# Kernel tuning notes

Measured on AMD Instinct MI355X. Metric: run time of the kernel, lower is better.

## Reference

```python
import jax, jax.numpy as jnp
import numpy as np

E = 500_000   # edges
N = 100_000   # nodes
Q = 256       # queries
N_REL = 200
R = 2 * N_REL + 1  # relation table rows (401)
D = 64        # in_dim
A = 64        # attn_dim
O = 64        # out_dim


def setup_inputs() -> dict:
    key = jax.random.key(0)
    ks = jax.random.split(key, 16)
    s = 1.0 / np.sqrt(D)
    # edges columns: [query_idx, head_ent, rel, tail_ent, sub_node, obj_node]
    col_q = jax.random.randint(ks[0], (E, 1), 0, Q)
    col_h = jax.random.randint(ks[1], (E, 1), 0, N)
    col_r = jax.random.randint(ks[2], (E, 1), 0, R)
    col_t = jax.random.randint(ks[3], (E, 1), 0, N)
    col_s = jax.random.randint(ks[4], (E, 1), 0, N)
    col_o = jax.random.randint(ks[5], (E, 1), 0, N)
    edges = jnp.concatenate([col_q, col_h, col_r, col_t, col_s, col_o], axis=1)
    return {
        "q_sub": jax.random.randint(ks[6], (Q,), 0, N),
        "q_emb": jax.random.normal(ks[7], (Q, D), dtype=jnp.float32),
        "rela_embed": jax.random.normal(ks[8], (R, D), dtype=jnp.float32),
        "hidden": jax.random.normal(ks[9], (N, D), dtype=jnp.float32),
        "edges": edges,
        "n_nodes": N,
        "Ws_W": jax.random.normal(ks[10], (A, D), dtype=jnp.float32) * s,
        "Ws_b": jnp.zeros((A,), dtype=jnp.float32),
        "Wr_W": jax.random.normal(ks[11], (A, D), dtype=jnp.float32) * s,
        "Wq_W": jax.random.normal(ks[12], (A, D), dtype=jnp.float32) * s,
        "Wqr_W": jax.random.normal(ks[13], (A, D), dtype=jnp.float32) * s,
        "wa_W": jax.random.normal(ks[14], (1, A), dtype=jnp.float32) * s,
        "wa_b": jnp.zeros((1,), dtype=jnp.float32),
        "Wh_W": jax.random.normal(ks[15], (O, D), dtype=jnp.float32) * s,
    }


def reference(q_sub, q_emb, rela_embed, hidden, edges, n_nodes,
              Ws_W, Ws_b, Wr_W, Wq_W, Wqr_W, wa_W, wa_b, Wh_W):
    # sample_flag == 0 path of GNNLayer.forward (use_lama_rel == 1, act = identity)
    sub = edges[:, 4]
    rel = edges[:, 2]
    obj = edges[:, 5]
    hs = hidden[sub]            # [E, D] gather
    hr = rela_embed[rel]        # [E, D] gather
    h_qr = q_emb[edges[:, 0]]   # [E, D] gather
    # attention MLP: sigmoid(w_alpha(ReLU(Ws hs + Wr hr + Wq hqr + Wqr (hr*hqr))))
    pre = (jnp.einsum('ed,ad->ea', hs, Ws_W) + Ws_b
           + jnp.einsum('ed,ad->ea', hr, Wr_W)
           + jnp.einsum('ed,ad->ea', h_qr, Wq_W)
           + jnp.einsum('ed,ad->ea', hr * h_qr, Wqr_W))
    alpha = jax.nn.sigmoid(jnp.einsum('ea,oa->eo', jax.nn.relu(pre), wa_W) + wa_b)  # [E,1]
    message = alpha * (hs * hr)                                # [E, D]
    message_agg = jax.ops.segment_sum(message, obj, num_segments=n_nodes)  # [N, D] scatter-sum
    hidden_new = jnp.einsum('nd,od->no', message_agg, Wh_W)    # act = identity
    return hidden_new, alpha
```

## Files before the change

kernel.cpp:

```cpp
#include <hip/hip_runtime.h>
#include <hip/hip_bf16.h>

#define EDGES  500000
#define NNODES 100000
#define QN     256
#define RN     401
#define DD     64
#define AA     64
#define OO     64

typedef __attribute__((ext_vector_type(8))) short short8;
typedef __attribute__((ext_vector_type(2))) short short2v;
typedef __attribute__((ext_vector_type(4))) float f32x4;
typedef __attribute__((ext_vector_type(2))) float f32x2;

__device__ inline unsigned short f2bf(float f) {
    union { float f; unsigned int u; } v; v.f = f;
    unsigned int u = v.u;
    u += 0x7FFFu + ((u >> 16) & 1u);
    return (unsigned short)(u >> 16);
}

__device__ inline f32x2 bfpair2f(unsigned int u) {
    union { unsigned int i; float f; } lo, hi;
    lo.i = u << 16;
    hi.i = u & 0xFFFF0000u;
    f32x2 r; r[0] = lo.f; r[1] = hi.f; return r;
}

__device__ inline short8 load8_cvt(const float* __restrict__ p) {
    f32x4 x0 = ((const f32x4*)p)[0];
    f32x4 x1 = ((const f32x4*)p)[1];
    short8 r;
    r[0] = (short)f2bf(x0[0]); r[1] = (short)f2bf(x0[1]);
    r[2] = (short)f2bf(x0[2]); r[3] = (short)f2bf(x0[3]);
    r[4] = (short)f2bf(x1[0]); r[5] = (short)f2bf(x1[1]);
    r[6] = (short)f2bf(x1[2]); r[7] = (short)f2bf(x1[3]);
    return r;
}

__device__ inline short8 load8_cvt_prod(const float* __restrict__ pa,
                                        const float* __restrict__ pb) {
    f32x4 a0 = ((const f32x4*)pa)[0];
    f32x4 a1 = ((const f32x4*)pa)[1];
    f32x4 b0 = ((const f32x4*)pb)[0];
    f32x4 b1 = ((const f32x4*)pb)[1];
    short8 r;
    r[0] = (short)f2bf(a0[0]*b0[0]); r[1] = (short)f2bf(a0[1]*b0[1]);
    r[2] = (short)f2bf(a0[2]*b0[2]); r[3] = (short)f2bf(a0[3]*b0[3]);
    r[4] = (short)f2bf(a1[0]*b1[0]); r[5] = (short)f2bf(a1[1]*b1[1]);
    r[6] = (short)f2bf(a1[2]*b1[2]); r[7] = (short)f2bf(a1[3]*b1[3]);
    return r;
}

__device__ inline void atomic_pk_add_bf16(short* addr, short2v v) {
#if __has_builtin(__builtin_amdgcn_global_atomic_fadd_v2bf16)
    __builtin_amdgcn_global_atomic_fadd_v2bf16(
        (__attribute__((address_space(1))) short2v*)addr, v);
#else
    asm volatile("global_atomic_pk_add_bf16 %0, %1, off"
                 :: "v"(addr), "v"(v) : "memory");
#endif
}

__global__ void k_xs(const float* __restrict__ hidden,
                     const float* __restrict__ Ws_W,
                     short* __restrict__ Xs,
                     short* __restrict__ hidden_bf) {
    __shared__ short W[AA * 72];
    int tid = threadIdx.x;
    for (int idx = tid; idx < AA * DD; idx += 256) {
        int a = idx >> 6, d = idx & 63;
        W[a * 72 + d] = (short)f2bf(Ws_W[idx]);
    }
    __syncthreads();
    int wave = tid >> 6, lane = tid & 63;
    int quad = lane >> 4, l15 = lane & 15;
    int rowbase = blockIdx.x * 64 + wave * 16;
    int row_a = rowbase + l15;

    f32x4 acc[4];
    for (int t = 0; t < 4; ++t) { acc[t][0]=acc[t][1]=acc[t][2]=acc[t][3]=0.f; }

#pragma unroll
    for (int ks = 0; ks < 2; ++ks) {
        int ka = ks * 32 + quad * 8;
        short8 afrag;
        if (row_a < NNODES) {
            afrag = load8_cvt(hidden + (size_t)row_a * DD + ka);
            *(short8*)(hidden_bf + (size_t)row_a * DD + ka) = afrag;
        } else {
            afrag = short8{0,0,0,0,0,0,0,0};
        }
#pragma unroll
        for (int t = 0; t < 4; ++t) {
            short8 bfrag = *(const short8*)&W[(t * 16 + l15) * 72 + ka];
            acc[t] = __builtin_amdgcn_mfma_f32_16x16x32_bf16(afrag, bfrag, acc[t], 0, 0, 0);
        }
    }
#pragma unroll
    for (int t = 0; t < 4; ++t)
#pragma unroll
        for (int r = 0; r < 4; ++r) {
            int row = rowbase + quad * 4 + r;
            if (row < NNODES) Xs[(size_t)row * AA + t * 16 + l15] = (short)f2bf(acc[t][r]);
        }
}

__global__ void k_p(const float* __restrict__ q_emb,
                    const float* __restrict__ rela,
                    const float* __restrict__ Wq_W,
                    const float* __restrict__ Wr_W,
                    const float* __restrict__ Wqr_W,
                    const float* __restrict__ Ws_b,
                    short* __restrict__ P) {
    __shared__ short W[AA * 200];
    int tid = threadIdx.x;
    for (int idx = tid; idx < AA * 192; idx += 256) {
        int a = idx / 192, k = idx - a * 192;
        float v = (k < 64) ? Wq_W[a * 64 + k]
                : (k < 128) ? Wr_W[a * 64 + (k - 64)]
                            : Wqr_W[a * 64 + (k - 128)];
        W[a * 200 + k] = (short)f2bf(v);
    }
    __syncthreads();
    int wave = tid >> 6, lane = tid & 63;
    int quad = lane >> 4, l15 = lane & 15;
    int pairbase = blockIdx.x * 64 + wave * 16;
    int mypair = pairbase + l15;
    int q = mypair / RN;
    int r = mypair - q * RN;
    const float* hq = q_emb + (size_t)q * DD;
    const float* hr = rela  + (size_t)r * DD;

    f32x4 acc[4];
#pragma unroll
    for (int t = 0; t < 4; ++t) {
        float b = Ws_b[t * 16 + l15];
        acc[t][0] = acc[t][1] = acc[t][2] = acc[t][3] = b;
    }

#pragma unroll
    for (int ks = 0; ks < 6; ++ks) {
        int ka = ks * 32 + quad * 8;
        short8 afrag;
        if (ka < 64)       afrag = load8_cvt(hq + ka);
        else if (ka < 128) afrag = load8_cvt(hr + (ka - 64));
        else               afrag = load8_cvt_prod(hq + (ka - 128), hr + (ka - 128));
#pragma unroll
        for (int t = 0; t < 4; ++t) {
            short8 bfrag = *(const short8*)&W[(t * 16 + l15) * 200 + ka];
            acc[t] = __builtin_amdgcn_mfma_f32_16x16x32_bf16(afrag, bfrag, acc[t], 0, 0, 0);
        }
    }
#pragma unroll
    for (int t = 0; t < 4; ++t)
#pragma unroll
        for (int rg = 0; rg < 4; ++rg) {
            int row = pairbase + quad * 4 + rg;
            P[(size_t)row * AA + t * 16 + l15] = (short)f2bf(acc[t][rg]);
        }
}

__global__ void k_edge(const int* __restrict__ edges,
                       const short* __restrict__ Xs,
                       const short* __restrict__ P,
                       const short* __restrict__ hidden_bf,
                       const float* __restrict__ rela,
                       const float* __restrict__ wa_W,
                       const float* __restrict__ wa_b,
                       short* __restrict__ agg,
                       float* __restrict__ alpha_out) {
    int tid  = threadIdx.x;
    int wave = tid >> 6, lane = tid & 63;
    int l32  = lane & 31;
    int half = lane >> 5;
    size_t e = (size_t)blockIdx.x * 8 + wave * 2 + half;

    const int* ep = edges + e * 6;
    int q = ep[0];
    int r = ep[2];
    int2 so = *(const int2*)&ep[4];
    int sub = so.x, obj = so.y;

    int c2 = 2 * l32;
    unsigned int xs_u = *(const unsigned int*)&Xs[(size_t)sub * AA + c2];
    unsigned int pp_u = *(const unsigned int*)&P[((size_t)q * RN + r) * AA + c2];
    f32x2 xs = bfpair2f(xs_u);
    f32x2 pp = bfpair2f(pp_u);
    f32x2 wa = *(const f32x2*)&wa_W[c2];

    float v = fmaxf(xs[0] + pp[0], 0.f) * wa[0]
            + fmaxf(xs[1] + pp[1], 0.f) * wa[1];
#pragma unroll
    for (int off = 16; off > 0; off >>= 1) v += __shfl_xor(v, off, 64);
    float alpha = 1.f / (1.f + __expf(-(v + wa_b[0])));
    if (l32 == 0) alpha_out[e] = alpha;

    unsigned int hs_u = *(const unsigned int*)&hidden_bf[(size_t)sub * DD + c2];
    f32x2 hs = bfpair2f(hs_u);
    f32x2 hr = *(const f32x2*)&rela[(size_t)r * DD + c2];
    short2v m;
    m[0] = (short)f2bf(alpha * hs[0] * hr[0]);
    m[1] = (short)f2bf(alpha * hs[1] * hr[1]);
    atomic_pk_add_bf16((short*)agg + (size_t)obj * DD + c2, m);
}

__global__ void k_out(const short* __restrict__ agg,
                      const float* __restrict__ Wh_W,
                      float* __restrict__ out) {
    __shared__ short W[OO * 72];
    int tid = threadIdx.x;
    for (int idx = tid; idx < OO * DD; idx += 256) {
        int o = idx >> 6, d = idx & 63;
        W[o * 72 + d] = (short)f2bf(Wh_W[idx]);
    }
    __syncthreads();
    int wave = tid >> 6, lane = tid & 63;
    int quad = lane >> 4, l15 = lane & 15;
    int rowbase = blockIdx.x * 64 + wave * 16;
    int row_a = rowbase + l15;

    f32x4 acc[4];
    for (int t = 0; t < 4; ++t) { acc[t][0]=acc[t][1]=acc[t][2]=acc[t][3]=0.f; }

#pragma unroll
    for (int ks = 0; ks < 2; ++ks) {
        int ka = ks * 32 + quad * 8;
        short8 afrag;
        if (row_a < NNODES) afrag = *(const short8*)(agg + (size_t)row_a * DD + ka);
        else                afrag = short8{0,0,0,0,0,0,0,0};
#pragma unroll
        for (int t = 0; t < 4; ++t) {
            short8 bfrag = *(const short8*)&W[(t * 16 + l15) * 72 + ka];
            acc[t] = __builtin_amdgcn_mfma_f32_16x16x32_bf16(afrag, bfrag, acc[t], 0, 0, 0);
        }
    }
#pragma unroll
    for (int t = 0; t < 4; ++t)
#pragma unroll
        for (int r = 0; r < 4; ++r) {
            int row = rowbase + quad * 4 + r;
            if (row < NNODES) out[(size_t)row * OO + t * 16 + l15] = acc[t][r];
        }
}

extern "C" void kernel_launch(void* const* d_in, const int* in_sizes, int n_in,
                              void* d_out, int out_size, void* d_ws, size_t ws_size,
                              hipStream_t stream) {
    const float* q_emb  = (const float*)d_in[1];
    const float* rela   = (const float*)d_in[2];
    const float* hidden = (const float*)d_in[3];
    const int*   edges  = (const int*)d_in[4];
    const float* Ws_W   = (const float*)d_in[6];
    const float* Ws_b   = (const float*)d_in[7];
    const float* Wr_W   = (const float*)d_in[8];
    const float* Wq_W   = (const float*)d_in[9];
    const float* Wqr_W  = (const float*)d_in[10];
    const float* wa_W   = (const float*)d_in[11];
    const float* wa_b   = (const float*)d_in[12];
    const float* Wh_W   = (const float*)d_in[13];

    short* Xs        = (short*)d_ws;
    short* P         = Xs + (size_t)NNODES * AA;
    short* hidden_bf = P + (size_t)QN * RN * AA;
    short* agg       = hidden_bf + (size_t)NNODES * DD;

    float* out       = (float*)d_out;
    float* alpha_out = out + (size_t)NNODES * OO;

    (void)hipMemsetAsync(agg, 0, (size_t)NNODES * DD * sizeof(short), stream);

    k_xs<<<(NNODES + 63) / 64, 256, 0, stream>>>(hidden, Ws_W, Xs, hidden_bf);
    k_p <<<(QN * RN) / 64, 256, 0, stream>>>(q_emb, rela, Wq_W, Wr_W, Wqr_W, Ws_b, P);
    k_edge<<<EDGES / 8, 256, 0, stream>>>(edges, Xs, P, hidden_bf, rela, wa_W, wa_b,
                                          agg, alpha_out);
    k_out<<<(NNODES + 63) / 64, 256, 0, stream>>>(agg, Wh_W, out);
}
```

Baseline: 213.8 us.

## Replace bf16 atomic scatter with counting-sort CSR and per-node gather aggregation

Builds a destination-sorted edge list every call (histogram, two-level scan, atomic scatter), then assigns one half-wave per destination node to accumulate messages in fp32 registers and write agg once. This removes 500K packed bf16 global atomics and the agg memset, and accumulates in higher precision. It adds four extra kernel launches, scattered random index reads through sorted_eid, and load imbalance from variable node degree, including a serial dependent loop per node.

```diff
diff --git a/kernel.cpp b/kernel.cpp
--- a/kernel.cpp
+++ b/kernel.cpp
@@ -8,9 +8,10 @@
 #define DD     64
 #define AA     64
 #define OO     64
+#define NB     391
+#define EB     1954
 
 typedef __attribute__((ext_vector_type(8))) short short8;
-typedef __attribute__((ext_vector_type(2))) short short2v;
 typedef __attribute__((ext_vector_type(4))) float f32x4;
 typedef __attribute__((ext_vector_type(2))) float f32x2;
 
@@ -51,16 +52,6 @@
     r[4] = (short)f2bf(a1[0]*b1[0]); r[5] = (short)f2bf(a1[1]*b1[1]);
     r[6] = (short)f2bf(a1[2]*b1[2]); r[7] = (short)f2bf(a1[3]*b1[3]);
     return r;
-}
-
-__device__ inline void atomic_pk_add_bf16(short* addr, short2v v) {
-#if __has_builtin(__builtin_amdgcn_global_atomic_fadd_v2bf16)
-    __builtin_amdgcn_global_atomic_fadd_v2bf16(
-        (__attribute__((address_space(1))) short2v*)addr, v);
-#else
-    asm volatile("global_atomic_pk_add_bf16 %0, %1, off"
-                 :: "v"(addr), "v"(v) : "memory");
-#endif
 }
 
 __global__ void k_xs(const float* __restrict__ hidden,
@@ -162,48 +153,102 @@
         }
 }
 
-__global__ void k_edge(const int* __restrict__ edges,
-                       const short* __restrict__ Xs,
-                       const short* __restrict__ P,
-                       const short* __restrict__ hidden_bf,
-                       const float* __restrict__ rela,
-                       const float* __restrict__ wa_W,
-                       const float* __restrict__ wa_b,
-                       short* __restrict__ agg,
-                       float* __restrict__ alpha_out) {
-    int tid  = threadIdx.x;
-    int wave = tid >> 6, lane = tid & 63;
-    int l32  = lane & 31;
-    int half = lane >> 5;
-    size_t e = (size_t)blockIdx.x * 8 + wave * 2 + half;
-
-    const int* ep = edges + e * 6;
-    int q = ep[0];
-    int r = ep[2];
-    int2 so = *(const int2*)&ep[4];
-    int sub = so.x, obj = so.y;
-
+__global__ void s1_hist(const int* __restrict__ edges, unsigned* __restrict__ cnt) {
+    int e = blockIdx.x * 256 + threadIdx.x;
+    if (e < EDGES) atomicAdd(&cnt[edges[(size_t)e * 6 + 5]], 1u);
+}
+
+__global__ void s2a_scan(const unsigned* __restrict__ cnt,
+                         unsigned* __restrict__ start_local,
+                         unsigned* __restrict__ cursor,
+                         unsigned* __restrict__ bsum) {
+    __shared__ unsigned sm[256];
+    int t = threadIdx.x;
+    int i = blockIdx.x * 256 + t;
+    unsigned v = (i < NNODES) ? cnt[i] : 0u;
+    sm[t] = v;
+    __syncthreads();
+    for (int off = 1; off < 256; off <<= 1) {
+        unsigned u = (t >= off) ? sm[t - off] : 0u;
+        __syncthreads();
+        sm[t] += u;
+        __syncthreads();
+    }
+    unsigned excl = sm[t] - v;
+    if (i < NNODES) { start_local[i] = excl; cursor[i] = excl; }
+    if (t == 255) bsum[blockIdx.x] = sm[255];
+}
+
+__global__ void s2b_scan(unsigned* __restrict__ bsum) {
+    __shared__ unsigned sm[512];
+    int t = threadIdx.x;
+    unsigned v = (t < NB) ? bsum[t] : 0u;
+    sm[t] = v;
+    __syncthreads();
+    for (int off = 1; off < 512; off <<= 1) {
+        unsigned u = (t >= off) ? sm[t - off] : 0u;
+        __syncthreads();
+        sm[t] += u;
+        __syncthreads();
+    }
+    if (t < NB) bsum[t] = sm[t] - v;
+}
+
+__global__ void s3_scatter(const int* __restrict__ edges,
+                           unsigned* __restrict__ cursor,
+                           const unsigned* __restrict__ bsum,
+                           unsigned* __restrict__ sorted_eid) {
+    int e = blockIdx.x * 256 + threadIdx.x;
+    if (e >= EDGES) return;
+    int obj = edges[(size_t)e * 6 + 5];
+    unsigned p = atomicAdd(&cursor[obj], 1u) + bsum[obj >> 8];
+    sorted_eid[p] = (unsigned)e;
+}
+
+__global__ void k_agg(const unsigned* __restrict__ sorted_eid,
+                      const unsigned* __restrict__ start_local,
+                      const unsigned* __restrict__ bsum,
+                      const unsigned* __restrict__ cnt,
+                      const int* __restrict__ edges,
+                      const short* __restrict__ Xs,
+                      const short* __restrict__ P,
+                      const short* __restrict__ hidden_bf,
+                      const float* __restrict__ rela,
+                      const float* __restrict__ wa_W,
+                      const float* __restrict__ wa_b,
+                      short* __restrict__ agg,
+                      float* __restrict__ alpha_out) {
+    int tid = threadIdx.x;
+    int l32 = tid & 31;
+    int n = blockIdx.x * 8 + (tid >> 5);
     int c2 = 2 * l32;
-    unsigned int xs_u = *(const unsigned int*)&Xs[(size_t)sub * AA + c2];
-    unsigned int pp_u = *(const unsigned int*)&P[((size_t)q * RN + r) * AA + c2];
-    f32x2 xs = bfpair2f(xs_u);
-    f32x2 pp = bfpair2f(pp_u);
+    unsigned base = start_local[n] + bsum[n >> 8];
+    unsigned num = cnt[n];
+    float wab = wa_b[0];
     f32x2 wa = *(const f32x2*)&wa_W[c2];
-
-    float v = fmaxf(xs[0] + pp[0], 0.f) * wa[0]
-            + fmaxf(xs[1] + pp[1], 0.f) * wa[1];
-#pragma unroll
-    for (int off = 16; off > 0; off >>= 1) v += __shfl_xor(v, off, 64);
-    float alpha = 1.f / (1.f + __expf(-(v + wa_b[0])));
-    if (l32 == 0) alpha_out[e] = alpha;
-
-    unsigned int hs_u = *(const unsigned int*)&hidden_bf[(size_t)sub * DD + c2];
-    f32x2 hs = bfpair2f(hs_u);
-    f32x2 hr = *(const f32x2*)&rela[(size_t)r * DD + c2];
-    short2v m;
-    m[0] = (short)f2bf(alpha * hs[0] * hr[0]);
-    m[1] = (short)f2bf(alpha * hs[1] * hr[1]);
-    atomic_pk_add_bf16((short*)agg + (size_t)obj * DD + c2, m);
+    float a0 = 0.f, a1 = 0.f;
+    for (unsigned j = 0; j < num; ++j) {
+        unsigned e = sorted_eid[base + j];
+        const int* ep = edges + (size_t)e * 6;
+        int q = ep[0], r = ep[2], sub = ep[4];
+        unsigned xs_u = *(const unsigned*)&Xs[(size_t)sub * AA + c2];
+        unsigned pp_u = *(const unsigned*)&P[((size_t)q * RN + r) * AA + c2];
+        f32x2 xs = bfpair2f(xs_u), pp = bfpair2f(pp_u);
+        float v = fmaxf(xs[0] + pp[0], 0.f) * wa[0]
+                + fmaxf(xs[1] + pp[1], 0.f) * wa[1];
+#pragma unroll
+        for (int off = 16; off > 0; off >>= 1) v += __shfl_xor(v, off, 64);
+        float alpha = 1.f / (1.f + __expf(-(v + wab)));
+        if (l32 == 0) alpha_out[e] = alpha;
+        unsigned hs_u = *(const unsigned*)&hidden_bf[(size_t)sub * DD + c2];
+        f32x2 hs = bfpair2f(hs_u);
+        f32x2 hr = *(const f32x2*)&rela[(size_t)r * DD + c2];
+        a0 += alpha * hs[0] * hr[0];
+        a1 += alpha * hs[1] * hr[1];
+    }
+    unsigned packed = (unsigned)(unsigned short)f2bf(a0)
+                    | ((unsigned)f2bf(a1) << 16);
+    *(unsigned*)&agg[(size_t)n * DD + c2] = packed;
 }
 
 __global__ void k_out(const short* __restrict__ agg,
@@ -265,15 +310,27 @@
     short* P         = Xs + (size_t)NNODES * AA;
     short* hidden_bf = P + (size_t)QN * RN * AA;
     short* agg       = hidden_bf + (size_t)NNODES * DD;
+    unsigned* cnt         = (unsigned*)(agg + (size_t)NNODES * DD);
+    unsigned* start_local = cnt + NNODES;
+    unsigned* cursor      = start_local + NNODES;
+    unsigned* bsum        = cursor + NNODES;
+    unsigned* sorted_eid  = bsum + 512;
 
     float* out       = (float*)d_out;
     float* alpha_out = out + (size_t)NNODES * OO;
 
-    (void)hipMemsetAsync(agg, 0, (size_t)NNODES * DD * sizeof(short), stream);
+    (void)hipMemsetAsync(cnt, 0, (size_t)NNODES * sizeof(unsigned), stream);
+
+    s1_hist   <<<EB, 256, 0, stream>>>(edges, cnt);
+    s2a_scan  <<<NB, 256, 0, stream>>>(cnt, start_local, cursor, bsum);
+    s2b_scan  <<<1, 512, 0, stream>>>(bsum);
+    s3_scatter<<<EB, 256, 0, stream>>>(edges, cursor, bsum, sorted_eid);
 
     k_xs<<<(NNODES + 63) / 64, 256, 0, stream>>>(hidden, Ws_W, Xs, hidden_bf);
     k_p <<<(QN * RN) / 64, 256, 0, stream>>>(q_emb, rela, Wq_W, Wr_W, Wqr_W, Ws_b, P);
-    k_edge<<<EDGES / 8, 256, 0, stream>>>(edges, Xs, P, hidden_bf, rela, wa_W, wa_b,
+
+    k_agg<<<NNODES / 8, 256, 0, stream>>>(sorted_eid, start_local, bsum, cnt, edges,
+                                          Xs, P, hidden_bf, rela, wa_W, wa_b,
                                           agg, alpha_out);
     k_out<<<(NNODES + 63) / 64, 256, 0, stream>>>(agg, Wh_W, out);
 }
```

After: 284.1 us. 1.33x slower.
